# Kernel tuning notes

Hardware: AMD Instinct MI355X
Metric: run time of the kernel (lower is better)

The kernel has to match this reference:

```python
import jax, jax.numpy as jnp
import numpy as np
import math

HEAD_DIM = 128
LAMBDA_INIT = 0.8
GN_EPS = 1e-05
NEG = -1e9


def ghostmax(scores):
    # softmax with an extra implicit zero logit (softmax-plus-one)
    m = jnp.maximum(jnp.max(scores, axis=-1, keepdims=True), 0.0)
    e = jnp.exp(scores - m)
    return e / (jnp.sum(e, axis=-1, keepdims=True) + jnp.exp(-m))


def setup_inputs() -> dict:
    key = jax.random.key(0)
    ks = jax.random.split(key, 8)
    B, H2, H, S, D = 2, 16, 8, 2048, HEAD_DIM
    return {
        "q": jax.random.normal(ks[0], (B, H2, S, D), dtype=jnp.float32),
        "k": jax.random.normal(ks[1], (B, H2, S, D), dtype=jnp.float32),
        "v": jax.random.normal(ks[2], (B, H, S, D), dtype=jnp.float32),
        "lambda_q1": 0.1 * jax.random.normal(ks[3], (D,), dtype=jnp.float32),
        "lambda_k1": 0.1 * jax.random.normal(ks[4], (D,), dtype=jnp.float32),
        "lambda_q2": 0.1 * jax.random.normal(ks[5], (D,), dtype=jnp.float32),
        "lambda_k2": 0.1 * jax.random.normal(ks[6], (D,), dtype=jnp.float32),
        "gn_weight": jnp.ones((H * D,), dtype=jnp.float32),
        "gn_bias": jnp.zeros((H * D,), dtype=jnp.float32),
    }


def reference(q, k, v, lambda_q1, lambda_k1, lambda_q2, lambda_k2, gn_weight, gn_bias):
    B, H2, S, D = q.shape
    H = H2 // 2
    scaling = 1.0 / math.sqrt(D)
    # [B, 2H, S, S] attention scores
    scores = jnp.einsum("bhsd,bhtd->bhst", q, k) * scaling
    causal_mask = jnp.triu(jnp.full((S, S), NEG, dtype=scores.dtype), k=1)
    scores = scores + causal_mask[None, None]
    w = ghostmax(scores)
    w = w.reshape(B, H, 2, S, S)
    lam = (
        jnp.exp(jnp.sum(lambda_q1 * lambda_k1))
        - jnp.exp(jnp.sum(lambda_q2 * lambda_k2))
        + LAMBDA_INIT
    )
    w = w[:, :, 0] - lam * w[:, :, 1]  # [B, H, S, S]
    out = jnp.einsum("bhst,bhtd->bhsd", w, v)  # [B, H, S, D]
    # torch .reshape(B, -1, S): raw row-major reinterpretation
    out = out.reshape(B, H * D, S)
    # GroupNorm: num_groups=H over channels H*D, normalized over (group channels, seq)
    g = out.reshape(B, H, D * S)
    mean = jnp.mean(g, axis=-1, keepdims=True)
    var = jnp.var(g, axis=-1, keepdims=True)
    g = (g - mean) * jax.lax.rsqrt(var + GN_EPS)
    out = g.reshape(B, H * D, S) * gn_weight[None, :, None] + gn_bias[None, :, None]
    return out * (1.0 - LAMBDA_INIT)
```

## Files before the change

### kernel.cpp

```cpp
#include <hip/hip_runtime.h>
#include <hip/hip_bf16.h>
#include <cstddef>
#include <cstdint>


typedef __bf16 bf16x8 __attribute__((ext_vector_type(8)));
typedef __bf16 bf16x4 __attribute__((ext_vector_type(4)));
typedef float f32x4 __attribute__((ext_vector_type(4)));

constexpr int SEQ = 2048;
constexpr int DH  = 128;
constexpr int NH  = 8;
constexpr int NH2 = 16;
constexpr float SCALE  = 0.088388347648318447f;
constexpr float QSCALE = 0.127517430f;

template <bool B> struct BoolK { static constexpr bool value = B; };

constexpr size_t QK_ELEMS = (size_t)2 * NH2 * SEQ * DH;
constexpr size_t V_ELEMS  = (size_t)2 * NH  * SEQ * DH;
constexpr size_t OFF_KB   = 4096;
constexpr size_t OFF_VT   = OFF_KB + QK_ELEMS * 2;
constexpr size_t WS_NEED  = OFF_VT + V_ELEMS * 2;

__device__ __forceinline__ void load_lds16(const void* g, void* l) {
  __builtin_amdgcn_global_load_lds(
      (const __attribute__((address_space(1))) uint32_t*)g,
      (__attribute__((address_space(3))) uint32_t*)l, 16, 0, 0);
}

__device__ __forceinline__ bf16x8 cvt8(float4 a, float4 b) {
  bf16x8 r;
  r[0] = (__bf16)a.x; r[1] = (__bf16)a.y; r[2] = (__bf16)a.z; r[3] = (__bf16)a.w;
  r[4] = (__bf16)b.x; r[5] = (__bf16)b.y; r[6] = (__bf16)b.z; r[7] = (__bf16)b.w;
  return r;
}

__global__ __launch_bounds__(256) void prep_kernel(
    const float* __restrict__ k, const float* __restrict__ v,
    __bf16* __restrict__ Kb, __bf16* __restrict__ Vtb,
    float* __restrict__ stats)
{
  __shared__ float tile[32][33];
  const int id = blockIdx.x;
  if (id == 0 && threadIdx.x < 64) stats[threadIdx.x] = 0.f;
  if (id < 4096) {
    const size_t i = ((size_t)id * 256 + threadIdx.x) * 8;
    float4 a = *(const float4*)(k + i);
    float4 b = *(const float4*)(k + i + 4);
    *(bf16x8*)(Kb + i) = cvt8(a, b);
  } else {
    const int vid = id - 4096;
    const int tt = vid & 63, dt = (vid >> 6) & 3, bh = vid >> 8;
    const int tr = threadIdx.x >> 3, tc = (threadIdx.x & 7) * 4;
    const float* src = v + ((size_t)bh * SEQ + tt * 32) * DH + dt * 32;
    float4 f = *(const float4*)(src + (size_t)tr * DH + tc);
    tile[tr][tc + 0] = f.x; tile[tr][tc + 1] = f.y;
    tile[tr][tc + 2] = f.z; tile[tr][tc + 3] = f.w;
    __syncthreads();
    __bf16* dst = Vtb + ((size_t)bh * DH + dt * 32 + tr) * SEQ + tt * 32 + tc;
    bf16x4 o;
    o[0] = (__bf16)tile[tc + 0][tr];
    o[1] = (__bf16)tile[tc + 1][tr];
    o[2] = (__bf16)tile[tc + 2][tr];
    o[3] = (__bf16)tile[tc + 3][tr];
    *(bf16x4*)dst = o;
  }
}

__global__ __launch_bounds__(512, 1) void attn3_kernel(
    const float* __restrict__ Qf, const __bf16* __restrict__ Kb,
    const __bf16* __restrict__ Vtb,
    const float* __restrict__ lq1, const float* __restrict__ lk1,
    const float* __restrict__ lq2, const float* __restrict__ lk2,
    float* __restrict__ Obuf, float* __restrict__ stats)
{
  __shared__ __align__(16) __bf16 ldsK[2][2][2][32][128];
  __shared__ __align__(16) __bf16 ldsVt[2][2][128][32];
  __shared__ __align__(16) __bf16 ldsP[2][4][2][16][36];
  __shared__ float ldsL[4][2][16];

  const int qt = 31 - (int)(blockIdx.x >> 4);
  const int bh = blockIdx.x & 15;
  const int b = bh >> 3, h = bh & 7;
  const int tid = threadIdx.x;
  const int g  = tid >> 8;
  const int t2 = tid & 255;
  const int w = t2 >> 6, lane = tid & 63;
  const int l15 = lane & 15, quad = lane >> 4;

  float a1 = lq1[lane]*lk1[lane] + lq1[lane+64]*lk1[lane+64];
  float a2 = lq2[lane]*lk2[lane] + lq2[lane+64]*lk2[lane+64];
  #pragma unroll
  for (int off = 1; off < 64; off <<= 1) {
    a1 += __shfl_xor(a1, off);
    a2 += __shfl_xor(a2, off);
  }
  const float lam = __expf(a1) - __expf(a2) + 0.8f;

  const size_t headQK = (size_t)(b*NH2 + 2*h) * SEQ * DH;
  const float*  Qh  = Qf + headQK;
  const __bf16* Kh  = Kb + headQK;
  const __bf16* Vth = Vtb + (size_t)(b*NH + h) * DH * SEQ;

  size_t goffK[4];
  #pragma unroll
  for (int i = 0; i < 4; ++i) {
    const int R  = w*16 + i*4 + quad;
    const int sh = R >> 5, kr = R & 31;
    const int cs = lane & 15;
    goffK[i] = ((size_t)sh * SEQ + kr) * DH + ((cs ^ (kr & 15)) * 8);
  }
  size_t goffV[2];
  #pragma unroll
  for (int i = 0; i < 2; ++i) {
    const int d  = w*32 + i*16 + ((t2 & 63) >> 2);
    const int cs = lane & 3;
    goffV[i] = (size_t)d * SEQ + ((cs ^ (d & 3)) * 8);
  }

  __bf16* ldsKg = &ldsK[g][0][0][0][0];
  __bf16* ldsVg = &ldsVt[g][0][0][0];

  const int qb = qt * 64;
  const int nph = qt + 1;

  const int qrow = qb + w*16 + l15;
  bf16x8 qf[2][4];
  #pragma unroll
  for (int sh = 0; sh < 2; ++sh) {
    const float* src = Qh + (size_t)sh*SEQ*DH + (size_t)qrow*DH + quad*8;
    #pragma unroll
    for (int kd = 0; kd < 4; ++kd) {
      float4 f0 = *(const float4*)(src + kd*32);
      float4 f1 = *(const float4*)(src + kd*32 + 4);
      f0.x *= QSCALE; f0.y *= QSCALE; f0.z *= QSCALE; f0.w *= QSCALE;
      f1.x *= QSCALE; f1.y *= QSCALE; f1.z *= QSCALE; f1.w *= QSCALE;
      qf[sh][kd] = cvt8(f0, f1);
    }
  }

  f32x4 oacc[2][8];
  float lsum[2][4];
  #pragma unroll
  for (int sh = 0; sh < 2; ++sh) {
    #pragma unroll
    for (int nt = 0; nt < 8; ++nt) oacc[sh][nt] = (f32x4){0.f,0.f,0.f,0.f};
    #pragma unroll
    for (int r = 0; r < 4; ++r) lsum[sh][r] = 0.f;
  }

  {
    const __bf16* kg = Kh + (size_t)g * 32 * DH;
    #pragma unroll
    for (int i = 0; i < 4; ++i)
      load_lds16(kg + goffK[i], ldsKg + w*2048 + i*512);
    const __bf16* vg = Vth + g * 32;
    #pragma unroll
    for (int i = 0; i < 2; ++i)
      load_lds16(vg + goffV[i], ldsVg + w*1024 + i*512);
  }
  __syncthreads();

  for (int j = 0; j < nph; ++j) {
    const int cur = j & 1;
    const int kbt = (2*j + g) * 32;

    if (j + 1 < nph) {
      const int nxt = cur ^ 1;
      const __bf16* kg = Kh + (size_t)(kbt + 64) * DH;
      #pragma unroll
      for (int i = 0; i < 4; ++i)
        load_lds16(kg + goffK[i], ldsKg + (size_t)nxt*8192 + w*2048 + i*512);
      const __bf16* vg = Vth + (kbt + 64);
      #pragma unroll
      for (int i = 0; i < 2; ++i)
        load_lds16(vg + goffV[i], ldsVg + (size_t)nxt*4096 + w*1024 + i*512);
    }

    f32x4 sacc[2][2];
    #pragma unroll
    for (int sh = 0; sh < 2; ++sh)
      #pragma unroll
      for (int n = 0; n < 2; ++n)
        sacc[sh][n] = (f32x4){0.f,0.f,0.f,0.f};
    __builtin_amdgcn_s_setprio(1);
    #pragma unroll
    for (int sh = 0; sh < 2; ++sh)
      #pragma unroll
      for (int n = 0; n < 2; ++n)
        #pragma unroll
        for (int kd = 0; kd < 4; ++kd) {
          bf16x8 kf = *(const bf16x8*)&ldsK[g][cur][sh][n*16 + l15][((kd*4 + quad) ^ l15) * 8];
          sacc[sh][n] = __builtin_amdgcn_mfma_f32_16x16x32_bf16(qf[sh][kd], kf, sacc[sh][n], 0, 0, 0);
        }
    __builtin_amdgcn_s_setprio(0);

    const int qrow0 = qb + w*16 + quad*4;
    auto sm_body = [&](auto MASKC) {
      constexpr bool MASKED = decltype(MASKC)::value;
      #pragma unroll
      for (int sh = 0; sh < 2; ++sh)
        #pragma unroll
        for (int r = 0; r < 4; ++r) {
          float p0 = __builtin_amdgcn_exp2f(sacc[sh][0][r]);
          float p1 = __builtin_amdgcn_exp2f(sacc[sh][1][r]);
          if constexpr (MASKED) {
            const int qr = qrow0 + r;
            if (kbt + l15      > qr) p0 = 0.f;
            if (kbt + l15 + 16 > qr) p1 = 0.f;
          }
          lsum[sh][r] += p0 + p1;
          ldsP[g][w][sh][quad*4 + r][l15]      = (__bf16)p0;
          ldsP[g][w][sh][quad*4 + r][l15 + 16] = (__bf16)p1;
        }
    };
    if (kbt + 31 <= qb + w*16) sm_body(BoolK<false>{});
    else                       sm_body(BoolK<true>{});

    {
      bf16x8 pf0 = *(const bf16x8*)&ldsP[g][w][0][l15][quad*8];
      bf16x8 pf1 = *(const bf16x8*)&ldsP[g][w][1][l15][quad*8];
      __builtin_amdgcn_s_setprio(1);
      #pragma unroll
      for (int nt = 0; nt < 8; ++nt) {
        bf16x8 vf = *(const bf16x8*)&ldsVt[g][cur][nt*16 + l15][(quad ^ (l15 & 3)) * 8];
        oacc[0][nt] = __builtin_amdgcn_mfma_f32_16x16x32_bf16(pf0, vf, oacc[0][nt], 0, 0, 0);
        oacc[1][nt] = __builtin_amdgcn_mfma_f32_16x16x32_bf16(pf1, vf, oacc[1][nt], 0, 0, 0);
      }
      __builtin_amdgcn_s_setprio(0);
    }
    __syncthreads();
  }

  float lr[2][4];
  #pragma unroll
  for (int sh = 0; sh < 2; ++sh)
    #pragma unroll
    for (int r = 0; r < 4; ++r) {
      float vsum = lsum[sh][r];
      #pragma unroll
      for (int off = 1; off < 16; off <<= 1) vsum += __shfl_xor(vsum, off);
      lr[sh][r] = vsum;
    }

  float* Oscr = (float*)&ldsK[0][0][0][0][0];
  if (g == 1) {
    #pragma unroll
    for (int sh = 0; sh < 2; ++sh)
      #pragma unroll
      for (int nt = 0; nt < 8; ++nt)
        #pragma unroll
        for (int r = 0; r < 4; ++r)
          Oscr[((w*2 + sh)*16 + quad*4 + r)*128 + nt*16 + l15] = oacc[sh][nt][r];
    if (l15 == 0) {
      #pragma unroll
      for (int sh = 0; sh < 2; ++sh)
        #pragma unroll
        for (int r = 0; r < 4; ++r)
          ldsL[w][sh][quad*4 + r] = lr[sh][r];
    }
  }
  __syncthreads();

  if (g == 0) {
    const int qrow0 = qb + w*16 + quad*4;
    float* obase = Obuf + (size_t)(b*NH + h) * SEQ * DH;
    float sum = 0.f, ss = 0.f;
    #pragma unroll
    for (int r = 0; r < 4; ++r) {
      const float l0 = lr[0][r] + ldsL[w][0][quad*4 + r] + 1.0f;
      const float l1 = lr[1][r] + ldsL[w][1][quad*4 + r] + 1.0f;
      const float i0 = 1.0f / l0;
      const float i1 = lam / l1;
      float* orow = obase + (size_t)(qrow0 + r) * DH + l15;
      #pragma unroll
      for (int nt = 0; nt < 8; ++nt) {
        const float o0 = oacc[0][nt][r] + Oscr[((w*2 + 0)*16 + quad*4 + r)*128 + nt*16 + l15];
        const float o1 = oacc[1][nt][r] + Oscr[((w*2 + 1)*16 + quad*4 + r)*128 + nt*16 + l15];
        const float val = o0 * i0 - o1 * i1;
        orow[nt*16] = val;
        sum += val;
        ss  += val * val;
      }
    }
    #pragma unroll
    for (int off = 1; off < 64; off <<= 1) {
      sum += __shfl_xor(sum, off);
      ss  += __shfl_xor(ss, off);
    }
    if (lane == 0) {
      atomicAdd(&stats[2*(b*NH + h)],     sum);
      atomicAdd(&stats[2*(b*NH + h) + 1], ss);
    }
  }
}

__global__ __launch_bounds__(256) void attn_fb_kernel(
    const float* __restrict__ q, const float* __restrict__ k,
    const float* __restrict__ v,
    const float* __restrict__ lq1, const float* __restrict__ lk1,
    const float* __restrict__ lq2, const float* __restrict__ lk2,
    float* __restrict__ Obuf, float* __restrict__ stats)
{
  __shared__ __align__(16) __bf16 lds_k[2][32][136];
  __shared__ __align__(16) __bf16 lds_vt[128][40];
  __shared__ __align__(16) __bf16 lds_p[4][2][16][40];

  const int qt = blockIdx.x, h = blockIdx.y, b = blockIdx.z;
  const int qb = qt * 64;
  const int tid = threadIdx.x;
  const int w = tid >> 6, lane = tid & 63;
  const int l15 = lane & 15, quad = lane >> 4;

  float a1 = lq1[lane]*lk1[lane] + lq1[lane+64]*lk1[lane+64];
  float a2 = lq2[lane]*lk2[lane] + lq2[lane+64]*lk2[lane+64];
  #pragma unroll
  for (int off = 1; off < 64; off <<= 1) {
    a1 += __shfl_xor(a1, off);
    a2 += __shfl_xor(a2, off);
  }
  const float lam = __expf(a1) - __expf(a2) + 0.8f;

  const float* qh0 = q + (size_t)(b*NH2 + 2*h) * SEQ * DH;
  const float* qh1 = qh0 + (size_t)SEQ * DH;
  const float* kh0 = k + (size_t)(b*NH2 + 2*h) * SEQ * DH;
  const float* kh1 = kh0 + (size_t)SEQ * DH;
  const float* vh  = v + (size_t)(b*NH + h) * SEQ * DH;

  bf16x8 qf[2][4];
  {
    const int qrow = qb + w*16 + l15;
    #pragma unroll
    for (int sh = 0; sh < 2; ++sh) {
      const float* src = (sh ? qh1 : qh0) + (size_t)qrow * DH + quad*8;
      #pragma unroll
      for (int kd = 0; kd < 4; ++kd) {
        float4 f0 = *(const float4*)(src + kd*32);
        float4 f1 = *(const float4*)(src + kd*32 + 4);
        qf[sh][kd] = cvt8(f0, f1);
      }
    }
  }

  f32x4 oacc[2][8];
  #pragma unroll
  for (int sh = 0; sh < 2; ++sh)
    #pragma unroll
    for (int nt = 0; nt < 8; ++nt)
      oacc[sh][nt] = (f32x4){0.f,0.f,0.f,0.f};

  float mst[2][4] = {{0.f,0.f,0.f,0.f},{0.f,0.f,0.f,0.f}};
  float lst[2][4] = {{1.f,1.f,1.f,1.f},{1.f,1.f,1.f,1.f}};

  const int krow = tid >> 2, ksh = krow >> 5, kr = krow & 31;
  const int kd0 = (tid & 3) * 32;
  const float* ksrc0 = (ksh ? kh1 : kh0) + kd0;
  const int vt = tid >> 3, vd = (tid & 7) * 16;

  const int nsteps = (qb + 64) / 32;
  for (int st = 0; st < nsteps; ++st) {
    const int kbt = st * 32;
    {
      const float* sp = ksrc0 + (size_t)(kbt + kr) * DH;
      #pragma unroll
      for (int c = 0; c < 4; ++c) {
        float4 f0 = *(const float4*)(sp + c*8);
        float4 f1 = *(const float4*)(sp + c*8 + 4);
        *(bf16x8*)&lds_k[ksh][kr][kd0 + c*8] = cvt8(f0, f1);
      }
      const float* vp = vh + (size_t)(kbt + vt) * DH + vd;
      #pragma unroll
      for (int c = 0; c < 4; ++c) {
        float4 f = *(const float4*)(vp + c*4);
        lds_vt[vd + c*4 + 0][vt] = (__bf16)f.x;
        lds_vt[vd + c*4 + 1][vt] = (__bf16)f.y;
        lds_vt[vd + c*4 + 2][vt] = (__bf16)f.z;
        lds_vt[vd + c*4 + 3][vt] = (__bf16)f.w;
      }
    }
    __syncthreads();

    f32x4 sacc[2][2];
    #pragma unroll
    for (int sh = 0; sh < 2; ++sh)
      #pragma unroll
      for (int n = 0; n < 2; ++n)
        sacc[sh][n] = (f32x4){0.f,0.f,0.f,0.f};

    #pragma unroll
    for (int sh = 0; sh < 2; ++sh)
      #pragma unroll
      for (int n = 0; n < 2; ++n)
        #pragma unroll
        for (int kd = 0; kd < 4; ++kd) {
          bf16x8 bf = *(const bf16x8*)&lds_k[sh][n*16 + l15][kd*32 + quad*8];
          sacc[sh][n] = __builtin_amdgcn_mfma_f32_16x16x32_bf16(qf[sh][kd], bf, sacc[sh][n], 0, 0, 0);
        }

    const int qrow0 = qb + w*16 + quad*4;
    const int c0 = kbt + l15, c1 = c0 + 16;
    #pragma unroll
    for (int sh = 0; sh < 2; ++sh) {
      #pragma unroll
      for (int r = 0; r < 4; ++r) {
        float s0 = sacc[sh][0][r] * SCALE;
        float s1 = sacc[sh][1][r] * SCALE;
        const int qr = qrow0 + r;
        if (c0 > qr) s0 = -1e30f;
        if (c1 > qr) s1 = -1e30f;
        float mx = fmaxf(s0, s1);
        #pragma unroll
        for (int off = 1; off < 16; off <<= 1)
          mx = fmaxf(mx, __shfl_xor(mx, off));
        const float mnew = fmaxf(mst[sh][r], mx);
        const float alpha = __expf(mst[sh][r] - mnew);
        mst[sh][r] = mnew;
        const float p0 = __expf(s0 - mnew);
        const float p1 = __expf(s1 - mnew);
        float rs = p0 + p1;
        #pragma unroll
        for (int off = 1; off < 16; off <<= 1)
          rs += __shfl_xor(rs, off);
        lst[sh][r] = lst[sh][r] * alpha + rs;
        #pragma unroll
        for (int nt = 0; nt < 8; ++nt)
          oacc[sh][nt][r] *= alpha;
        lds_p[w][sh][quad*4 + r][l15]      = (__bf16)p0;
        lds_p[w][sh][quad*4 + r][l15 + 16] = (__bf16)p1;
      }
    }

    {
      bf16x8 pf0 = *(const bf16x8*)&lds_p[w][0][l15][quad*8];
      bf16x8 pf1 = *(const bf16x8*)&lds_p[w][1][l15][quad*8];
      #pragma unroll
      for (int nt = 0; nt < 8; ++nt) {
        bf16x8 vf = *(const bf16x8*)&lds_vt[nt*16 + l15][quad*8];
        oacc[0][nt] = __builtin_amdgcn_mfma_f32_16x16x32_bf16(pf0, vf, oacc[0][nt], 0, 0, 0);
        oacc[1][nt] = __builtin_amdgcn_mfma_f32_16x16x32_bf16(pf1, vf, oacc[1][nt], 0, 0, 0);
      }
    }
    __syncthreads();
  }

  const int qrow0 = qb + w*16 + quad*4;
  float* obase = Obuf + (size_t)(b*NH + h) * SEQ * DH;
  float sum = 0.f, ss = 0.f;
  #pragma unroll
  for (int r = 0; r < 4; ++r) {
    const float i0 = 1.0f / lst[0][r];
    const float i1 = lam / lst[1][r];
    float* orow = obase + (size_t)(qrow0 + r) * DH + l15;
    #pragma unroll
    for (int nt = 0; nt < 8; ++nt) {
      const float val = oacc[0][nt][r] * i0 - oacc[1][nt][r] * i1;
      orow[nt*16] = val;
      sum += val;
      ss  += val * val;
    }
  }
  #pragma unroll
  for (int off = 1; off < 64; off <<= 1) {
    sum += __shfl_xor(sum, off);
    ss  += __shfl_xor(ss, off);
  }
  if (lane == 0) {
    atomicAdd(&stats[2*(b*NH + h)],     sum);
    atomicAdd(&stats[2*(b*NH + h) + 1], ss);
  }
}

__global__ __launch_bounds__(256) void norm_kernel(
    float* __restrict__ Obuf, const float* __restrict__ stats,
    const float* __restrict__ gw, const float* __restrict__ gb)
{
  const int idx = (blockIdx.x * 256 + threadIdx.x) * 4;
  const int bh = idx >> 18;
  const int local = idx & 262143;
  const float inv = 1.0f / 262144.0f;
  const float mean = stats[2*bh] * inv;
  const float var  = stats[2*bh + 1] * inv - mean * mean;
  const float rstd = rsqrtf(var + 1e-5f);
  const int c = ((bh & 7) << 7) + (local >> 11);
  const float wq = gw[c] * rstd;
  const float bq = gb[c];
  float4 o = *(const float4*)(Obuf + idx);
  float4 r;
  r.x = ((o.x - mean) * wq + bq) * 0.2f;
  r.y = ((o.y - mean) * wq + bq) * 0.2f;
  r.z = ((o.z - mean) * wq + bq) * 0.2f;
  r.w = ((o.w - mean) * wq + bq) * 0.2f;
  *(float4*)(Obuf + idx) = r;
}

extern "C" void kernel_launch(void* const* d_in, const int* in_sizes, int n_in,
                              void* d_out, int out_size, void* d_ws, size_t ws_size,
                              hipStream_t stream) {
  const float* q   = (const float*)d_in[0];
  const float* k   = (const float*)d_in[1];
  const float* v   = (const float*)d_in[2];
  const float* lq1 = (const float*)d_in[3];
  const float* lk1 = (const float*)d_in[4];
  const float* lq2 = (const float*)d_in[5];
  const float* lk2 = (const float*)d_in[6];
  const float* gw  = (const float*)d_in[7];
  const float* gb  = (const float*)d_in[8];
  float* out = (float*)d_out;
  float* stats = (float*)d_ws;

  if (ws_size >= WS_NEED) {
    __bf16* Kb  = (__bf16*)((char*)d_ws + OFF_KB);
    __bf16* Vtb = (__bf16*)((char*)d_ws + OFF_VT);

    prep_kernel<<<8192, 256, 0, stream>>>(k, v, Kb, Vtb, stats);

    attn3_kernel<<<512, 512, 0, stream>>>(q, Kb, Vtb,
        lq1, lk1, lq2, lk2, out, stats);
  } else {
    (void)hipMemsetAsync(d_ws, 0, 256, stream);
    attn_fb_kernel<<<dim3(32, NH, 2), 256, 0, stream>>>(q, k, v,
        lq1, lk1, lq2, lk2, out, stats);
  }

  const int total = 2 * NH * SEQ * DH;
  norm_kernel<<<total / 1024, 256, 0, stream>>>(out, stats, gw, gb);
}
```

Baseline: 204.7 us.

## Shrink LDS footprint and raise occupancy target for attention kernel

Single-buffers the K tile in LDS, adding a barrier between the QK MFMA phase and the next K prefetch. The P staging buffer loses its padding and uses a rotated column swizzle instead, and the row-sum exchange buffer is aliased into P. Launch bounds are raised to request four blocks per CU, and block-to-tile ordering now launches heavy tiles first and then light tiles ascending. The goal is to fit more blocks per CU to hide latency. The cost is an extra barrier per iteration, less K prefetch overlap, and a register cap that may cause spills given the large accumulator set.

```diff
diff --git a/kernel.cpp b/kernel.cpp
--- a/kernel.cpp
+++ b/kernel.cpp
@@ -68,20 +68,21 @@
   }
 }
 
-__global__ __launch_bounds__(512, 1) void attn3_kernel(
+__global__ __launch_bounds__(512, 4) void attn3_kernel(
     const float* __restrict__ Qf, const __bf16* __restrict__ Kb,
     const __bf16* __restrict__ Vtb,
     const float* __restrict__ lq1, const float* __restrict__ lk1,
     const float* __restrict__ lq2, const float* __restrict__ lk2,
     float* __restrict__ Obuf, float* __restrict__ stats)
 {
-  __shared__ __align__(16) __bf16 ldsK[2][2][2][32][128];
+  __shared__ __align__(16) __bf16 ldsK[2][2][32][128];
   __shared__ __align__(16) __bf16 ldsVt[2][2][128][32];
-  __shared__ __align__(16) __bf16 ldsP[2][4][2][16][36];
-  __shared__ float ldsL[4][2][16];
-
-  const int qt = 31 - (int)(blockIdx.x >> 4);
-  const int bh = blockIdx.x & 15;
+  __shared__ __align__(16) __bf16 ldsP[2][4][2][16][32];
+
+  const int bid = (int)blockIdx.x;
+  int qt, bh;
+  if (bid < 256) { qt = 31 - (bid >> 4); bh = bid & 15; }
+  else           { qt = (bid - 256) >> 4; bh = bid & 15; }
   const int b = bh >> 3, h = bh & 7;
   const int tid = threadIdx.x;
   const int g  = tid >> 8;
@@ -119,7 +120,7 @@
     goffV[i] = (size_t)d * SEQ + ((cs ^ (d & 3)) * 8);
   }
 
-  __bf16* ldsKg = &ldsK[g][0][0][0][0];
+  __bf16* ldsKg = &ldsK[g][0][0][0];
   __bf16* ldsVg = &ldsVt[g][0][0][0];
 
   const int qb = qt * 64;
@@ -150,6 +151,10 @@
     for (int r = 0; r < 4; ++r) lsum[sh][r] = 0.f;
   }
 
+  const int prot = ((quad + (l15 >> 2)) & 3) * 8;
+  const int pc0  = (l15 + quad*8) & 31;
+  const int pc1  = pc0 ^ 16;
+
   {
     const __bf16* kg = Kh + (size_t)g * 32 * DH;
     #pragma unroll
@@ -166,35 +171,37 @@
     const int cur = j & 1;
     const int kbt = (2*j + g) * 32;
 
+    f32x4 sacc[2][2];
+    #pragma unroll
+    for (int sh = 0; sh < 2; ++sh)
+      #pragma unroll
+      for (int n = 0; n < 2; ++n)
+        sacc[sh][n] = (f32x4){0.f,0.f,0.f,0.f};
+    __builtin_amdgcn_s_setprio(1);
+    #pragma unroll
+    for (int sh = 0; sh < 2; ++sh)
+      #pragma unroll
+      for (int n = 0; n < 2; ++n)
+        #pragma unroll
+        for (int kd = 0; kd < 4; ++kd) {
+          bf16x8 kf = *(const bf16x8*)&ldsK[g][sh][n*16 + l15][((kd*4 + quad) ^ l15) * 8];
+          sacc[sh][n] = __builtin_amdgcn_mfma_f32_16x16x32_bf16(qf[sh][kd], kf, sacc[sh][n], 0, 0, 0);
+        }
+    __builtin_amdgcn_s_setprio(0);
+
+    __syncthreads();
+
     if (j + 1 < nph) {
       const int nxt = cur ^ 1;
       const __bf16* kg = Kh + (size_t)(kbt + 64) * DH;
       #pragma unroll
       for (int i = 0; i < 4; ++i)
-        load_lds16(kg + goffK[i], ldsKg + (size_t)nxt*8192 + w*2048 + i*512);
+        load_lds16(kg + goffK[i], ldsKg + w*2048 + i*512);
       const __bf16* vg = Vth + (kbt + 64);
       #pragma unroll
       for (int i = 0; i < 2; ++i)
         load_lds16(vg + goffV[i], ldsVg + (size_t)nxt*4096 + w*1024 + i*512);
     }
-
-    f32x4 sacc[2][2];
-    #pragma unroll
-    for (int sh = 0; sh < 2; ++sh)
-      #pragma unroll
-      for (int n = 0; n < 2; ++n)
-        sacc[sh][n] = (f32x4){0.f,0.f,0.f,0.f};
-    __builtin_amdgcn_s_setprio(1);
-    #pragma unroll
-    for (int sh = 0; sh < 2; ++sh)
-      #pragma unroll
-      for (int n = 0; n < 2; ++n)
-        #pragma unroll
-        for (int kd = 0; kd < 4; ++kd) {
-          bf16x8 kf = *(const bf16x8*)&ldsK[g][cur][sh][n*16 + l15][((kd*4 + quad) ^ l15) * 8];
-          sacc[sh][n] = __builtin_amdgcn_mfma_f32_16x16x32_bf16(qf[sh][kd], kf, sacc[sh][n], 0, 0, 0);
-        }
-    __builtin_amdgcn_s_setprio(0);
 
     const int qrow0 = qb + w*16 + quad*4;
     auto sm_body = [&](auto MASKC) {
@@ -211,16 +218,16 @@
             if (kbt + l15 + 16 > qr) p1 = 0.f;
           }
           lsum[sh][r] += p0 + p1;
-          ldsP[g][w][sh][quad*4 + r][l15]      = (__bf16)p0;
-          ldsP[g][w][sh][quad*4 + r][l15 + 16] = (__bf16)p1;
+          ldsP[g][w][sh][quad*4 + r][pc0] = (__bf16)p0;
+          ldsP[g][w][sh][quad*4 + r][pc1] = (__bf16)p1;
         }
     };
     if (kbt + 31 <= qb + w*16) sm_body(BoolK<false>{});
     else                       sm_body(BoolK<true>{});
 
     {
-      bf16x8 pf0 = *(const bf16x8*)&ldsP[g][w][0][l15][quad*8];
-      bf16x8 pf1 = *(const bf16x8*)&ldsP[g][w][1][l15][quad*8];
+      bf16x8 pf0 = *(const bf16x8*)&ldsP[g][w][0][l15][prot];
+      bf16x8 pf1 = *(const bf16x8*)&ldsP[g][w][1][l15][prot];
       __builtin_amdgcn_s_setprio(1);
       #pragma unroll
       for (int nt = 0; nt < 8; ++nt) {
@@ -244,7 +251,8 @@
       lr[sh][r] = vsum;
     }
 
-  float* Oscr = (float*)&ldsK[0][0][0][0][0];
+  float* Oscr  = (float*)&ldsK[0][0][0][0];
+  float* ldsLa = (float*)&ldsP[0][0][0][0][0];
   if (g == 1) {
     #pragma unroll
     for (int sh = 0; sh < 2; ++sh)
@@ -258,7 +266,7 @@
       for (int sh = 0; sh < 2; ++sh)
         #pragma unroll
         for (int r = 0; r < 4; ++r)
-          ldsL[w][sh][quad*4 + r] = lr[sh][r];
+          ldsLa[(w*2 + sh)*16 + quad*4 + r] = lr[sh][r];
     }
   }
   __syncthreads();
@@ -269,8 +277,8 @@
     float sum = 0.f, ss = 0.f;
     #pragma unroll
     for (int r = 0; r < 4; ++r) {
-      const float l0 = lr[0][r] + ldsL[w][0][quad*4 + r] + 1.0f;
-      const float l1 = lr[1][r] + ldsL[w][1][quad*4 + r] + 1.0f;
+      const float l0 = lr[0][r] + ldsLa[(w*2 + 0)*16 + quad*4 + r] + 1.0f;
+      const float l1 = lr[1][r] + ldsLa[(w*2 + 1)*16 + quad*4 + r] + 1.0f;
       const float i0 = 1.0f / l0;
       const float i1 = lam / l1;
       float* orow = obase + (size_t)(qrow0 + r) * DH + l15;
```

Result: slower. 296.5 us (+44.8%).
